# Kernel tuning notes

Measured on AMD Instinct MI355X. Metric: run time of the kernel, lower is better.

The kernel has to match this reference:

```python
import jax, jax.numpy as jnp
import numpy as np

N = 50000       # nodes
E = 1000000     # edges
H = 128         # hidden_channels
M = 64          # middle_channels
NR, NS = 3, 7   # num_radial, num_spherical
F1 = NR * NS * NS  # 147
F2 = NR * NS       # 21
L = 3           # num_layers (residual lins)
OUT = 128       # output_channels
G = 512         # num graphs in batch
EPS = 1e-5


def swish(v):
    return v * jax.nn.sigmoid(v)


def setup_inputs() -> dict:
    key = jax.random.key(0)
    ks = jax.random.split(key, 24)
    s = 0.05
    w = lambda k, shp: jax.random.normal(k, shp, dtype=jnp.float32) * s
    return {
        "x": jax.random.normal(ks[0], (N, H), dtype=jnp.float32),
        "feature1": jax.random.uniform(ks[1], (E, F1), dtype=jnp.float32),
        "feature2": jax.random.uniform(ks[2], (E, F2), dtype=jnp.float32),
        "edge_index": jax.random.randint(ks[3], (2, E), 0, N),
        "batch": jnp.sort(jax.random.randint(ks[4], (N,), 0, G)),
        # params (stored as [in, out]; torch F.linear uses [out, in] -- same math)
        "lin_w": w(ks[5], (H, H)), "lin_b": jnp.zeros((H,), jnp.float32),
        "f1_w1": w(ks[6], (F1, M)), "f1_w2": w(ks[7], (M, H)),
        "f2_w1": w(ks[8], (F2, M)), "f2_w2": w(ks[9], (M, H)),
        "conv1_rel_w": w(ks[10], (H, H)), "conv1_rel_b": jnp.zeros((H,), jnp.float32),
        "conv1_root_w": w(ks[11], (H, H)),
        "conv2_rel_w": w(ks[12], (H, H)), "conv2_rel_b": jnp.zeros((H,), jnp.float32),
        "conv2_root_w": w(ks[13], (H, H)),
        "lin1_w": w(ks[14], (H, H)), "lin1_b": jnp.zeros((H,), jnp.float32),
        "lin2_w": w(ks[15], (H, H)), "lin2_b": jnp.zeros((H,), jnp.float32),
        "lincat_w": w(ks[16], (2 * H, H)), "lincat_b": jnp.zeros((H,), jnp.float32),
        "norm_w": jnp.ones((H,), jnp.float32), "norm_b": jnp.zeros((H,), jnp.float32),
        "norm_ms": jnp.ones((H,), jnp.float32),  # GraphNorm mean_scale
        "lins_w": w(ks[17], (L, H, H)), "lins_b": jnp.zeros((L, H), jnp.float32),
        "final_w": w(ks[18], (H, OUT)), "final_b": jnp.zeros((OUT,), jnp.float32),
    }


def reference(x, feature1, feature2, edge_index, batch,
              lin_w, lin_b, f1_w1, f1_w2, f2_w1, f2_w2,
              conv1_rel_w, conv1_rel_b, conv1_root_w,
              conv2_rel_w, conv2_rel_b, conv2_root_w,
              lin1_w, lin1_b, lin2_w, lin2_b, lincat_w, lincat_b,
              norm_w, norm_b, norm_ms, lins_w, lins_b, final_w, final_b):
    src, dst = edge_index[0], edge_index[1]  # message flows src -> dst

    xh = swish(x @ lin_w + lin_b)

    # TwoLayerLinear (act=False): two bias-free linears
    f1 = (feature1 @ f1_w1) @ f1_w2   # [E, H]
    f2 = (feature2 @ f2_w1) @ f2_w2   # [E, H]

    # EdgeGraphConv: scatter-add of edge_weight * x_j, then lin_rel + lin_root(x)
    agg1 = jax.ops.segment_sum(f1 * xh[src], dst, num_segments=N)
    c1 = agg1 @ conv1_rel_w + conv1_rel_b + xh @ conv1_root_w
    h1 = swish(c1 @ lin1_w + lin1_b)

    agg2 = jax.ops.segment_sum(f2 * xh[src], dst, num_segments=N)
    c2 = agg2 @ conv2_rel_w + conv2_rel_b + xh @ conv2_root_w
    h2 = swish(c2 @ lin2_w + lin2_b)

    h = jnp.concatenate([h1, h2], axis=1) @ lincat_w + lincat_b + xh
    for i in range(L):
        h = swish(h @ lins_w[i] + lins_b[i]) + h

    # GraphNorm over per-graph segments
    counts = jnp.maximum(
        jax.ops.segment_sum(jnp.ones((N, 1), h.dtype), batch, num_segments=G), 1.0)
    mean = jax.ops.segment_sum(h, batch, num_segments=G) / counts
    out = h - mean[batch] * norm_ms
    var = jax.ops.segment_sum(out * out, batch, num_segments=G) / counts
    inv_std = jax.lax.rsqrt(var + EPS)
    h = norm_w * out * inv_std[batch] + norm_b

    return h @ final_w + final_b
```

## Files before the change

kernel.cpp:

```cpp
#include <hip/hip_runtime.h>
#include <hip/hip_bf16.h>
#include <stdint.h>

typedef __bf16 bf16x8 __attribute__((ext_vector_type(8)));
typedef float  f32x4  __attribute__((ext_vector_type(4)));

#define MFMA16(a, b, c) __builtin_amdgcn_mfma_f32_16x16x32_bf16((a), (b), (c), 0, 0, 0)

__global__ __launch_bounds__(256) void node_gemm(
    const void* __restrict__ A0, int a0f, const void* __restrict__ A1v, int a1f,
    const float* __restrict__ W0, const float* __restrict__ W1,
    const float* __restrict__ bias, const void* __restrict__ resv, int resf,
    void* __restrict__ outv, int outf, int nrows, int do_swish)
{
    extern __shared__ char smem[];
    const int K  = A1v ? 256 : 128;
    const int KP = K + 8;
    __bf16* WT = (__bf16*)smem;
    int tid = threadIdx.x;

    for (int i = tid; i < 16384; i += 256) { int k = i >> 7, n = i & 127; WT[n * KP + k] = (__bf16)W0[i]; }
    if (W1)
        for (int i = tid; i < 16384; i += 256) { int k = i >> 7, n = i & 127; WT[n * KP + 128 + k] = (__bf16)W1[i]; }
    __syncthreads();

    int wave = tid >> 6, lane = tid & 63, m = lane & 15, q = lane >> 4, kg = q * 8;
    int rowA = blockIdx.x * 64 + wave * 16 + m;
    if (rowA >= nrows) rowA = nrows - 1;

    f32x4 acc[8];
#pragma unroll
    for (int i = 0; i < 8; ++i) acc[i] = (f32x4){0.f, 0.f, 0.f, 0.f};

    for (int k0 = 0; k0 < K; k0 += 32) {
        int kk = k0 + kg;
        const void* Ap = A0; int isf = a0f; int ko = kk;
        if (kk >= 128) { Ap = A1v; isf = a1f; ko = kk - 128; }
        bf16x8 af;
        if (isf) {
            const float* p = (const float*)Ap + (size_t)rowA * 128 + ko;
            f32x4 u0 = *(const f32x4*)p;
            f32x4 u1 = *(const f32x4*)(p + 4);
#pragma unroll
            for (int j = 0; j < 4; ++j) { af[j] = (__bf16)u0[j]; af[4 + j] = (__bf16)u1[j]; }
        } else {
            af = *(const bf16x8*)((const __bf16*)Ap + (size_t)rowA * 128 + ko);
        }
#pragma unroll
        for (int ct = 0; ct < 8; ++ct) {
            bf16x8 bfr = *(const bf16x8*)(WT + (ct * 16 + m) * KP + kk);
            acc[ct] = MFMA16(af, bfr, acc[ct]);
        }
    }

    int rb = blockIdx.x * 64 + wave * 16 + q * 4;
#pragma unroll
    for (int ct = 0; ct < 8; ++ct) {
        int col = ct * 16 + m;
        float bb = bias ? bias[col] : 0.f;
#pragma unroll
        for (int rg = 0; rg < 4; ++rg) {
            int r = rb + rg;
            if (r < nrows) {
                float v = acc[ct][rg] + bb;
                if (do_swish) v = v / (1.f + __expf(-v));
                if (resv) v += resf ? ((const float*)resv)[(size_t)r * 128 + col]
                                    : (float)((const __bf16*)resv)[(size_t)r * 128 + col];
                if (outf) ((float*)outv)[(size_t)r * 128 + col] = v;
                else      ((__bf16*)outv)[(size_t)r * 128 + col] = (__bf16)v;
            }
        }
    }
}

template <int KF, int K32, int AST>
__global__ __launch_bounds__(256) void edge_conv(
    const float* __restrict__ feat, const float* __restrict__ W1g,
    const float* __restrict__ W2g, const __bf16* __restrict__ xh,
    const int* __restrict__ eidx, float* __restrict__ agg, int E_)
{
    extern __shared__ char smem[];
    __bf16* A1  = (__bf16*)smem;
    __bf16* WT1 = (__bf16*)(smem + 128 * AST * 2);
    __bf16* T1L = (__bf16*)smem;
    __bf16* XHL = (__bf16*)(smem + 18432);
    __bf16* WT2 = (__bf16*)(smem + 18432 + 34816);
    int* sSrc = (int*)(smem + 71680);
    int* sDst = sSrc + 128;

    int tid = threadIdx.x;
    int e0  = blockIdx.x * 128;

    if (tid < 128) {
        int e = e0 + tid, s = 0, d = -1;
        if (e < E_) { s = eidx[e]; d = eidx[E_ + e]; }
        sSrc[tid] = s; sDst[tid] = d;
    }

    const float* fp = feat + (size_t)e0 * KF;
    int valid;
    {
        long rem = ((long)E_ - e0) * (long)KF;
        valid = rem > (long)(128 * KF) ? 128 * KF : (rem < 0 ? 0 : (int)rem);
    }
    for (int i = tid; i < 128 * KF; i += 256) {
        int r = i / KF, c = i - r * KF;
        float v = (i < valid) ? fp[i] : 0.f;
        A1[r * AST + c] = (__bf16)v;
    }
    for (int i = tid; i < 128 * (K32 - KF); i += 256) {
        int r = i / (K32 - KF), c = KF + i - r * (K32 - KF);
        ((unsigned short*)A1)[r * AST + c] = 0;
    }
    for (int i = tid; i < KF * 64; i += 256) { int k = i >> 6, n = i & 63; WT1[n * AST + k] = (__bf16)W1g[i]; }
    for (int i = tid; i < 64 * (K32 - KF); i += 256) {
        int n = i / (K32 - KF), k = KF + i - n * (K32 - KF);
        ((unsigned short*)WT1)[n * AST + k] = 0;
    }
    __syncthreads();

    int wave = tid >> 6, lane = tid & 63, m = lane & 15, q = lane >> 4, kg = q * 8;

    f32x4 accT[2][4];
#pragma unroll
    for (int a = 0; a < 2; ++a)
#pragma unroll
        for (int b = 0; b < 4; ++b) accT[a][b] = (f32x4){0.f, 0.f, 0.f, 0.f};
#pragma unroll
    for (int k0 = 0; k0 < K32; k0 += 32) {
        bf16x8 a0 = *(const bf16x8*)(A1 + (wave * 32 + m) * AST + k0 + kg);
        bf16x8 a1 = *(const bf16x8*)(A1 + (wave * 32 + 16 + m) * AST + k0 + kg);
#pragma unroll
        for (int ct = 0; ct < 4; ++ct) {
            bf16x8 b = *(const bf16x8*)(WT1 + (ct * 16 + m) * AST + k0 + kg);
            accT[0][ct] = MFMA16(a0, b, accT[0][ct]);
            accT[1][ct] = MFMA16(a1, b, accT[1][ct]);
        }
    }
    __syncthreads();

#pragma unroll
    for (int rt = 0; rt < 2; ++rt)
#pragma unroll
        for (int ct = 0; ct < 4; ++ct)
#pragma unroll
            for (int rg = 0; rg < 4; ++rg) {
                int row = wave * 32 + rt * 16 + q * 4 + rg;
                int col = ct * 16 + m;
                T1L[row * 72 + col] = (__bf16)accT[rt][ct][rg];
            }
    for (int i2 = tid; i2 < 128 * 16; i2 += 256) {
        int r = i2 >> 4, c8 = (i2 & 15) * 8;
        *(bf16x8*)(XHL + r * 136 + c8) = *(const bf16x8*)(xh + (size_t)sSrc[r] * 128 + c8);
    }
    for (int i = tid; i < 64 * 128; i += 256) { int k = i >> 7, n = i & 127; WT2[n * 72 + k] = (__bf16)W2g[i]; }
    __syncthreads();

    f32x4 acc2[2][8];
#pragma unroll
    for (int a = 0; a < 2; ++a)
#pragma unroll
        for (int b = 0; b < 8; ++b) acc2[a][b] = (f32x4){0.f, 0.f, 0.f, 0.f};
#pragma unroll
    for (int k0 = 0; k0 < 64; k0 += 32) {
        bf16x8 a0 = *(const bf16x8*)(T1L + (wave * 32 + m) * 72 + k0 + kg);
        bf16x8 a1 = *(const bf16x8*)(T1L + (wave * 32 + 16 + m) * 72 + k0 + kg);
#pragma unroll
        for (int ct = 0; ct < 8; ++ct) {
            bf16x8 b = *(const bf16x8*)(WT2 + (ct * 16 + m) * 72 + k0 + kg);
            acc2[0][ct] = MFMA16(a0, b, acc2[0][ct]);
            acc2[1][ct] = MFMA16(a1, b, acc2[1][ct]);
        }
    }

#pragma unroll
    for (int rt = 0; rt < 2; ++rt) {
#pragma unroll
        for (int rg = 0; rg < 4; ++rg) {
            int rl = wave * 32 + rt * 16 + q * 4 + rg;
            int d = sDst[rl];
            if (d >= 0) {
                float* ap = agg + (size_t)d * 128;
#pragma unroll
                for (int ct = 0; ct < 8; ++ct) {
                    int col = ct * 16 + m;
                    float v = acc2[rt][ct][rg] * (float)XHL[rl * 136 + col];
                    unsafeAtomicAdd(ap + col, v);
                }
            }
        }
    }
}

__device__ inline int lb_search(const int* a, int n, int v)
{
    int lo = 0, hi = n;
    while (lo < hi) { int mid = (lo + hi) >> 1; if (a[mid] < v) lo = mid + 1; else hi = mid; }
    return lo;
}

__global__ __launch_bounds__(256) void graph_stats(
    const float* __restrict__ h, const int* __restrict__ batch,
    const float* __restrict__ norm_w, const float* __restrict__ norm_ms,
    float* __restrict__ meanms, float* __restrict__ scalev, int Nn)
{
    int g = blockIdx.x, tid = threadIdx.x;
    int s = lb_search(batch, Nn, g);
    int e = lb_search(batch, Nn, g + 1);
    __shared__ float r1[256], r2[256];
    int c = tid & 127, half = tid >> 7;
    float S1 = 0.f, S2 = 0.f;
    for (int r = s + half; r < e; r += 2) {
        float v = h[(size_t)r * 128 + c];
        S1 += v; S2 += v * v;
    }
    r1[tid] = S1; r2[tid] = S2;
    __syncthreads();
    if (tid < 128) {
        float s1 = r1[tid] + r1[tid + 128];
        float s2 = r2[tid] + r2[tid + 128];
        float cnt = (float)((e - s) > 0 ? (e - s) : 1);
        float mean = s1 / cnt, E2 = s2 / cnt;
        float msv = norm_ms[tid];
        float mm = mean * msv;
        float var = E2 - 2.f * mm * mean + mm * mm;
        meanms[g * 128 + tid] = mm;
        scalev[g * 128 + tid] = norm_w[tid] * rsqrtf(var + 1e-5f);
    }
}

__global__ __launch_bounds__(256) void final_kernel(
    const float* __restrict__ h, const int* __restrict__ batch,
    const float* __restrict__ meanms, const float* __restrict__ scalev,
    const float* __restrict__ norm_b, const float* __restrict__ Wf,
    const float* __restrict__ bfinal, float* __restrict__ out, int Nn)
{
    extern __shared__ char smem[];
    __bf16* WT = (__bf16*)smem;
    __bf16* AT = (__bf16*)(smem + 128 * 136 * 2);
    int tid = threadIdx.x;

    for (int i = tid; i < 16384; i += 256) { int k = i >> 7, n = i & 127; WT[n * 136 + k] = (__bf16)Wf[i]; }
    int r0 = blockIdx.x * 64;
    for (int i = tid; i < 64 * 128; i += 256) {
        int r = i >> 7, c = i & 127, gr = r0 + r;
        float v = 0.f;
        if (gr < Nn) {
            int g = batch[gr];
            v = (h[(size_t)gr * 128 + c] - meanms[g * 128 + c]) * scalev[g * 128 + c] + norm_b[c];
        }
        AT[r * 136 + c] = (__bf16)v;
    }
    __syncthreads();

    int wave = tid >> 6, lane = tid & 63, m = lane & 15, q = lane >> 4, kg = q * 8;
    f32x4 acc[8];
#pragma unroll
    for (int i = 0; i < 8; ++i) acc[i] = (f32x4){0.f, 0.f, 0.f, 0.f};
    for (int k0 = 0; k0 < 128; k0 += 32) {
        bf16x8 a = *(const bf16x8*)(AT + (wave * 16 + m) * 136 + k0 + kg);
#pragma unroll
        for (int ct = 0; ct < 8; ++ct) {
            bf16x8 b = *(const bf16x8*)(WT + (ct * 16 + m) * 136 + k0 + kg);
            acc[ct] = MFMA16(a, b, acc[ct]);
        }
    }
    int rb = r0 + wave * 16 + q * 4;
#pragma unroll
    for (int ct = 0; ct < 8; ++ct) {
        int col = ct * 16 + m;
        float bb = bfinal[col];
#pragma unroll
        for (int rg = 0; rg < 4; ++rg) {
            int r = rb + rg;
            if (r < Nn) out[(size_t)r * 128 + col] = acc[ct][rg] + bb;
        }
    }
}

extern "C" void kernel_launch(void* const* d_in, const int* in_sizes, int n_in,
                              void* d_out, int out_size, void* d_ws, size_t ws_size,
                              hipStream_t stream)
{
    const int N = in_sizes[0] / 128;
    const int E = in_sizes[3] / 2;

    const float* x         = (const float*)d_in[0];
    const float* feat1     = (const float*)d_in[1];
    const float* feat2     = (const float*)d_in[2];
    const int*   eidx      = (const int*)d_in[3];
    const int*   batch     = (const int*)d_in[4];
    const float* lin_w     = (const float*)d_in[5];
    const float* lin_b     = (const float*)d_in[6];
    const float* f1_w1     = (const float*)d_in[7];
    const float* f1_w2     = (const float*)d_in[8];
    const float* f2_w1     = (const float*)d_in[9];
    const float* f2_w2     = (const float*)d_in[10];
    const float* c1_rel_w  = (const float*)d_in[11];
    const float* c1_rel_b  = (const float*)d_in[12];
    const float* c1_root_w = (const float*)d_in[13];
    const float* c2_rel_w  = (const float*)d_in[14];
    const float* c2_rel_b  = (const float*)d_in[15];
    const float* c2_root_w = (const float*)d_in[16];
    const float* lin1_w    = (const float*)d_in[17];
    const float* lin1_b    = (const float*)d_in[18];
    const float* lin2_w    = (const float*)d_in[19];
    const float* lin2_b    = (const float*)d_in[20];
    const float* lincat_w  = (const float*)d_in[21];
    const float* lincat_b  = (const float*)d_in[22];
    const float* norm_w    = (const float*)d_in[23];
    const float* norm_b    = (const float*)d_in[24];
    const float* norm_ms   = (const float*)d_in[25];
    const float* lins_w    = (const float*)d_in[26];
    const float* lins_b    = (const float*)d_in[27];
    const float* final_w   = (const float*)d_in[28];
    const float* final_b   = (const float*)d_in[29];

    char* ws = (char*)d_ws;
    size_t nh = (size_t)N * 128;
    __bf16* xh     = (__bf16*)ws;
    __bf16* cbuf   = (__bf16*)(ws + nh * 2);
    __bf16* h1     = (__bf16*)(ws + nh * 4);
    __bf16* h2     = (__bf16*)(ws + nh * 6);
    float*  meanms = (float*)(ws + nh * 8);
    float*  scalev = (float*)(ws + nh * 8 + 512 * 128 * 4);
    float*  aggh   = (float*)d_out;

    const int    nbN    = (N + 63) / 64;
    const int    nbE    = (E + 127) / 128;
    const size_t smemN1 = 136 * 128 * 2;
    const size_t smemN2 = 264 * 128 * 2;
    const size_t smemE  = 72704;
    const size_t smemF  = 128 * 136 * 2 + 64 * 136 * 2;

    hipFuncSetAttribute((const void*)node_gemm, hipFuncAttributeMaxDynamicSharedMemorySize, (int)smemN2);
    hipFuncSetAttribute((const void*)&edge_conv<147, 160, 168>, hipFuncAttributeMaxDynamicSharedMemorySize, (int)smemE);
    hipFuncSetAttribute((const void*)&edge_conv<21, 32, 40>, hipFuncAttributeMaxDynamicSharedMemorySize, (int)smemE);
    hipFuncSetAttribute((const void*)final_kernel, hipFuncAttributeMaxDynamicSharedMemorySize, (int)smemF);

    node_gemm<<<nbN, 256, smemN1, stream>>>(x, 1, nullptr, 0, lin_w, nullptr, lin_b,
                                            nullptr, 0, xh, 0, N, 1);
    hipMemsetAsync(aggh, 0, nh * 4, stream);
    edge_conv<147, 160, 168><<<nbE, 256, smemE, stream>>>(feat1, f1_w1, f1_w2, xh, eidx, aggh, E);
    node_gemm<<<nbN, 256, smemN2, stream>>>(aggh, 1, xh, 0, c1_rel_w, c1_root_w, c1_rel_b,
                                            nullptr, 0, cbuf, 0, N, 0);
    node_gemm<<<nbN, 256, smemN1, stream>>>(cbuf, 0, nullptr, 0, lin1_w, nullptr, lin1_b,
                                            nullptr, 0, h1, 0, N, 1);
    hipMemsetAsync(aggh, 0, nh * 4, stream);
    edge_conv<21, 32, 40><<<nbE, 256, smemE, stream>>>(feat2, f2_w1, f2_w2, xh, eidx, aggh, E);
    node_gemm<<<nbN, 256, smemN2, stream>>>(aggh, 1, xh, 0, c2_rel_w, c2_root_w, c2_rel_b,
                                            nullptr, 0, cbuf, 0, N, 0);
    node_gemm<<<nbN, 256, smemN1, stream>>>(cbuf, 0, nullptr, 0, lin2_w, nullptr, lin2_b,
                                            nullptr, 0, h2, 0, N, 1);
    node_gemm<<<nbN, 256, smemN2, stream>>>(h1, 0, h2, 0, lincat_w, lincat_w + 16384, lincat_b,
                                            xh, 0, aggh, 1, N, 0);
    for (int i = 0; i < 3; ++i)
        node_gemm<<<nbN, 256, smemN1, stream>>>(aggh, 1, nullptr, 0, lins_w + i * 16384, nullptr,
                                                lins_b + i * 128, aggh, 1, aggh, 1, N, 1);
    graph_stats<<<512, 256, 0, stream>>>(aggh, batch, norm_w, norm_ms, meanms, scalev, N);
    final_kernel<<<nbN, 256, smemF, stream>>>(aggh, batch, meanms, scalev, norm_b,
                                              final_w, final_b, aggh, N);
}
```

Measured before the change: 2.396 ms.

## Sort edges by destination and pre-reduce segments before atomic scatter

Adds a counting sort of edges by destination (histogram, single-block scan, atomic scatter) computed every call, then processes edges in sorted order. Edge features are gathered through the permutation, and the products are staged in shared memory so runs of equal destination are summed locally before one atomic per run per column. This replaces 128 atomics per edge with far fewer, but adds three preprocessing kernels, a slow single-block scan over the nodes, and uncoalesced row gathers of the edge feature matrices.

```diff
diff --git a/kernel.cpp b/kernel.cpp
--- a/kernel.cpp
+++ b/kernel.cpp
@@ -73,39 +73,88 @@
     }
 }
 
+__global__ __launch_bounds__(256) void k_hist(
+    const int* __restrict__ eidx, int* __restrict__ cnt, int E_)
+{
+    int e = blockIdx.x * 256 + threadIdx.x;
+    if (e < E_) atomicAdd(&cnt[eidx[E_ + e]], 1);
+}
+
+__global__ __launch_bounds__(1024) void k_scan(int* __restrict__ data, int n)
+{
+    __shared__ int wsum[16];
+    __shared__ int wbase[16];
+    __shared__ int carry_s;
+    int tid = threadIdx.x, lane = tid & 63, wid = tid >> 6;
+    if (tid == 0) carry_s = 0;
+    __syncthreads();
+    for (int base = 0; base < n; base += 1024) {
+        int i = base + tid;
+        int v = (i < n) ? data[i] : 0;
+        int s = v;
+#pragma unroll
+        for (int off = 1; off < 64; off <<= 1) {
+            int t = __shfl_up(s, off);
+            if (lane >= off) s += t;
+        }
+        if (lane == 63) wsum[wid] = s;
+        __syncthreads();
+        if (tid == 0) {
+            int acc = carry_s;
+#pragma unroll
+            for (int w = 0; w < 16; ++w) { wbase[w] = acc; acc += wsum[w]; }
+            carry_s = acc;
+        }
+        __syncthreads();
+        if (i < n) data[i] = wbase[wid] + s - v;
+        __syncthreads();
+    }
+}
+
+__global__ __launch_bounds__(256) void k_scatter(
+    const int* __restrict__ eidx, int* __restrict__ wptr,
+    int* __restrict__ sperm, int* __restrict__ ssrc, int* __restrict__ sdst, int E_)
+{
+    int e = blockIdx.x * 256 + threadIdx.x;
+    if (e < E_) {
+        int s = eidx[e], d = eidx[E_ + e];
+        int p = atomicAdd(&wptr[d], 1);
+        sperm[p] = e; ssrc[p] = s; sdst[p] = d;
+    }
+}
+
 template <int KF, int K32, int AST>
 __global__ __launch_bounds__(256) void edge_conv(
     const float* __restrict__ feat, const float* __restrict__ W1g,
     const float* __restrict__ W2g, const __bf16* __restrict__ xh,
-    const int* __restrict__ eidx, float* __restrict__ agg, int E_)
+    const int* __restrict__ sperm, const int* __restrict__ ssrc,
+    const int* __restrict__ sdst, float* __restrict__ agg, int E_)
 {
     extern __shared__ char smem[];
     __bf16* A1  = (__bf16*)smem;
     __bf16* WT1 = (__bf16*)(smem + 128 * AST * 2);
-    __bf16* T1L = (__bf16*)smem;
-    __bf16* XHL = (__bf16*)(smem + 18432);
-    __bf16* WT2 = (__bf16*)(smem + 18432 + 34816);
-    int* sSrc = (int*)(smem + 71680);
-    int* sDst = sSrc + 128;
+    __bf16* XHL = (__bf16*)smem;
+    __bf16* T1L = (__bf16*)(smem + 34816);
+    __bf16* WT2 = (__bf16*)(smem + 53248);
+    float*  MS  = (float*)(smem + 34816);
+    int* sP = (int*)(smem + 71680);
+    int* sS = sP + 128;
+    int* sD = sP + 256;
 
     int tid = threadIdx.x;
-    int e0  = blockIdx.x * 128;
+    int p0  = blockIdx.x * 128;
 
     if (tid < 128) {
-        int e = e0 + tid, s = 0, d = -1;
-        if (e < E_) { s = eidx[e]; d = eidx[E_ + e]; }
-        sSrc[tid] = s; sDst[tid] = d;
-    }
-
-    const float* fp = feat + (size_t)e0 * KF;
-    int valid;
-    {
-        long rem = ((long)E_ - e0) * (long)KF;
-        valid = rem > (long)(128 * KF) ? 128 * KF : (rem < 0 ? 0 : (int)rem);
-    }
+        int p = p0 + tid; int e = -1, s = 0, d = -1;
+        if (p < E_) { e = sperm[p]; s = ssrc[p]; d = sdst[p]; }
+        sP[tid] = e; sS[tid] = s; sD[tid] = d;
+    }
+    __syncthreads();
+
     for (int i = tid; i < 128 * KF; i += 256) {
         int r = i / KF, c = i - r * KF;
-        float v = (i < valid) ? fp[i] : 0.f;
+        int e = sP[r];
+        float v = (e >= 0) ? feat[(size_t)e * KF + c] : 0.f;
         A1[r * AST + c] = (__bf16)v;
     }
     for (int i = tid; i < 128 * (K32 - KF); i += 256) {
@@ -151,7 +200,7 @@
             }
     for (int i2 = tid; i2 < 128 * 16; i2 += 256) {
         int r = i2 >> 4, c8 = (i2 & 15) * 8;
-        *(bf16x8*)(XHL + r * 136 + c8) = *(const bf16x8*)(xh + (size_t)sSrc[r] * 128 + c8);
+        *(bf16x8*)(XHL + r * 136 + c8) = *(const bf16x8*)(xh + (size_t)sS[r] * 128 + c8);
     }
     for (int i = tid; i < 64 * 128; i += 256) { int k = i >> 7, n = i & 127; WT2[n * 72 + k] = (__bf16)W2g[i]; }
     __syncthreads();
@@ -172,23 +221,38 @@
             acc2[1][ct] = MFMA16(a1, b, acc2[1][ct]);
         }
     }
-
-#pragma unroll
-    for (int rt = 0; rt < 2; ++rt) {
-#pragma unroll
-        for (int rg = 0; rg < 4; ++rg) {
-            int rl = wave * 32 + rt * 16 + q * 4 + rg;
-            int d = sDst[rl];
-            if (d >= 0) {
-                float* ap = agg + (size_t)d * 128;
-#pragma unroll
-                for (int ct = 0; ct < 8; ++ct) {
+    __syncthreads();
+
+#pragma unroll
+    for (int half = 0; half < 2; ++half) {
+#pragma unroll
+        for (int rt = 0; rt < 2; ++rt)
+#pragma unroll
+            for (int c4 = 0; c4 < 4; ++c4) {
+                int ct = half * 4 + c4;
+#pragma unroll
+                for (int rg = 0; rg < 4; ++rg) {
+                    int row = wave * 32 + rt * 16 + q * 4 + rg;
                     int col = ct * 16 + m;
-                    float v = acc2[rt][ct][rg] * (float)XHL[rl * 136 + col];
-                    unsafeAtomicAdd(ap + col, v);
+                    MS[row * 68 + c4 * 16 + m] = acc2[rt][ct][rg] * (float)XHL[row * 136 + col];
                 }
             }
-        }
+        __syncthreads();
+        {
+            int c = tid & 63, seg = tid >> 6, r0 = seg * 32;
+            float ssum = 0.f;
+            int cur = sD[r0];
+            for (int r = r0; r < r0 + 32; ++r) {
+                int d = sD[r];
+                if (d != cur) {
+                    if (cur >= 0) unsafeAtomicAdd(agg + (size_t)cur * 128 + half * 64 + c, ssum);
+                    ssum = 0.f; cur = d;
+                }
+                ssum += MS[r * 68 + c];
+            }
+            if (cur >= 0) unsafeAtomicAdd(agg + (size_t)cur * 128 + half * 64 + c, ssum);
+        }
+        if (half == 0) __syncthreads();
     }
 }
 
@@ -324,13 +388,19 @@
     __bf16* h2     = (__bf16*)(ws + nh * 6);
     float*  meanms = (float*)(ws + nh * 8);
     float*  scalev = (float*)(ws + nh * 8 + 512 * 128 * 4);
+    char*   ip     = ws + nh * 8 + 512 * 128 * 4 * 2;
+    int* wptr  = (int*)ip;
+    int* sperm = (int*)(ip + (size_t)N * 4);
+    int* ssrc  = (int*)(ip + (size_t)N * 4 + (size_t)E * 4);
+    int* sdst  = (int*)(ip + (size_t)N * 4 + (size_t)E * 8);
     float*  aggh   = (float*)d_out;
 
     const int    nbN    = (N + 63) / 64;
     const int    nbE    = (E + 127) / 128;
+    const int    nbES   = (E + 255) / 256;
     const size_t smemN1 = 136 * 128 * 2;
     const size_t smemN2 = 264 * 128 * 2;
-    const size_t smemE  = 72704;
+    const size_t smemE  = 73216;
     const size_t smemF  = 128 * 136 * 2 + 64 * 136 * 2;
 
     hipFuncSetAttribute((const void*)node_gemm, hipFuncAttributeMaxDynamicSharedMemorySize, (int)smemN2);
@@ -338,16 +408,23 @@
     hipFuncSetAttribute((const void*)&edge_conv<21, 32, 40>, hipFuncAttributeMaxDynamicSharedMemorySize, (int)smemE);
     hipFuncSetAttribute((const void*)final_kernel, hipFuncAttributeMaxDynamicSharedMemorySize, (int)smemF);
 
+    hipMemsetAsync(wptr, 0, (size_t)N * 4, stream);
+    k_hist<<<nbES, 256, 0, stream>>>(eidx, wptr, E);
+    k_scan<<<1, 1024, 0, stream>>>(wptr, N);
+    k_scatter<<<nbES, 256, 0, stream>>>(eidx, wptr, sperm, ssrc, sdst, E);
+
     node_gemm<<<nbN, 256, smemN1, stream>>>(x, 1, nullptr, 0, lin_w, nullptr, lin_b,
                                             nullptr, 0, xh, 0, N, 1);
     hipMemsetAsync(aggh, 0, nh * 4, stream);
-    edge_conv<147, 160, 168><<<nbE, 256, smemE, stream>>>(feat1, f1_w1, f1_w2, xh, eidx, aggh, E);
+    edge_conv<147, 160, 168><<<nbE, 256, smemE, stream>>>(feat1, f1_w1, f1_w2, xh,
+                                                          sperm, ssrc, sdst, aggh, E);
     node_gemm<<<nbN, 256, smemN2, stream>>>(aggh, 1, xh, 0, c1_rel_w, c1_root_w, c1_rel_b,
                                             nullptr, 0, cbuf, 0, N, 0);
     node_gemm<<<nbN, 256, smemN1, stream>>>(cbuf, 0, nullptr, 0, lin1_w, nullptr, lin1_b,
                                             nullptr, 0, h1, 0, N, 1);
     hipMemsetAsync(aggh, 0, nh * 4, stream);
-    edge_conv<21, 32, 40><<<nbE, 256, smemE, stream>>>(feat2, f2_w1, f2_w2, xh, eidx, aggh, E);
+    edge_conv<21, 32, 40><<<nbE, 256, smemE, stream>>>(feat2, f2_w1, f2_w2, xh,
+                                                       sperm, ssrc, sdst, aggh, E);
     node_gemm<<<nbN, 256, smemN2, stream>>>(aggh, 1, xh, 0, c2_rel_w, c2_root_w, c2_rel_b,
                                             nullptr, 0, cbuf, 0, N, 0);
     node_gemm<<<nbN, 256, smemN1, stream>>>(cbuf, 0, nullptr, 0, lin2_w, nullptr, lin2_b,
```

Result: faster. 2.320 ms (-3.2%).
